# Performance work log

Hardware: AMD Instinct MI355X
Metric: run time of the kernel (lower is better)

Reference implementation:

```python
import jax, jax.numpy as jnp
import numpy as np

B, S, D, H = 2, 2048, 1024, 16
DK = D // H


def setup_inputs() -> dict:
    key = jax.random.key(0)
    ks = jax.random.split(key, 12)
    lim = 1.0 / np.sqrt(D)
    def lin(kw, kb):
        W = jax.random.uniform(kw, (D, D), jnp.float32, -lim, lim)
        b = jax.random.uniform(kb, (D,), jnp.float32, -lim, lim)
        return W, b
    Wq, bq = lin(ks[0], ks[1])
    Wk, bk = lin(ks[2], ks[3])
    Wv, bv = lin(ks[4], ks[5])
    Wo, bo = lin(ks[6], ks[7])
    Q = jax.random.normal(ks[8], (B, S, D), jnp.float32)
    K = jax.random.normal(ks[9], (B, S, D), jnp.float32)
    V = jax.random.normal(ks[10], (B, S, D), jnp.float32)
    # causal mask, broadcastable to (B, H, S, S)
    mask = jnp.broadcast_to(jnp.tril(jnp.ones((S, S), jnp.bool_))[None, None], (B, 1, S, S))
    return {"Q": Q, "K": K, "V": V, "mask": mask,
            "Wq": Wq, "bq": bq, "Wk": Wk, "bk": bk,
            "Wv": Wv, "bv": bv, "Wo": Wo, "bo": bo}


def reference(Q, K, V, mask, Wq, bq, Wk, bk, Wv, bv, Wo, bo):
    def split(x):  # (B,S,D) -> (B,H,S,DK)
        return x.reshape(B, S, H, DK).transpose(0, 2, 1, 3)
    q = split(Q @ Wq.T + bq)
    k = split(K @ Wk.T + bk)
    v = split(V @ Wv.T + bv)
    scores = jnp.einsum('bhqd,bhkd->bhqk', q, k) / jnp.sqrt(jnp.float32(DK))
    scores = jnp.where(mask, scores, jnp.float32(-1e9))
    probs = jax.nn.softmax(scores, axis=-1)
    out = jnp.einsum('bhqk,bhkd->bhqd', probs, v)  # (B,H,S,DK)
    out = out.transpose(0, 2, 1, 3).reshape(B, S, D)
    return out @ Wo.T + bo
```

## Files before the change

kernel.cpp:

```cpp
#include <hip/hip_runtime.h>

#define S_LEN 2048
#define D_DIM 1024
#define H_NUM 16
#define DK_DIM 64
#define BATCH 2
#define M_TOT (BATCH * S_LEN)
#define XSZ 4194304
#define WSZ 1048576
#define SCALE_LOG2 0.18033688f

typedef __bf16 bf16x8 __attribute__((ext_vector_type(8)));
typedef float f32x4 __attribute__((ext_vector_type(4)));
typedef unsigned short u16;

__device__ inline u16 f2bf(float f) {
  union { float f; unsigned u; } v; v.f = f;
  unsigned u = v.u;
  return (u16)((u + 0x7FFFu + ((u >> 16) & 1u)) >> 16);
}

typedef const __attribute__((address_space(1))) unsigned int gu32;
typedef __attribute__((address_space(3))) unsigned int lu32;
__device__ inline void glds16(const u16* g, u16* l) {
  __builtin_amdgcn_global_load_lds((gu32*)g, (lu32*)l, 16, 0, 0);
}

__global__ __launch_bounds__(256)
void convert_kernel(const float* __restrict__ Q, const float* __restrict__ K,
                    const float* __restrict__ V, const float* __restrict__ Wq,
                    const float* __restrict__ Wk, const float* __restrict__ Wv,
                    const float* __restrict__ Wo, u16* __restrict__ Xb,
                    u16* __restrict__ Wb) {
  const size_t e = ((size_t)blockIdx.x * 256 + threadIdx.x) * 8;
  const float* src;
  u16* dst;
  size_t off;
  if (e < 3ull * XSZ) {
    const int a = (int)(e >> 22);
    src = (a == 0) ? Q : (a == 1) ? K : V;
    off = e - ((size_t)a << 22);
    dst = Xb + e;
  } else {
    const size_t ew = e - 3ull * XSZ;
    const int a = (int)(ew >> 20);
    src = (a == 0) ? Wq : (a == 1) ? Wk : (a == 2) ? Wv : Wo;
    off = ew - ((size_t)a << 20);
    dst = Wb + ew;
  }
  const float4 v0 = *reinterpret_cast<const float4*>(&src[off]);
  const float4 v1 = *reinterpret_cast<const float4*>(&src[off + 4]);
  ushort4 w0, w1;
  w0.x = f2bf(v0.x); w0.y = f2bf(v0.y); w0.z = f2bf(v0.z); w0.w = f2bf(v0.w);
  w1.x = f2bf(v1.x); w1.y = f2bf(v1.y); w1.z = f2bf(v1.z); w1.w = f2bf(v1.w);
  *reinterpret_cast<ushort4*>(dst) = w0;
  *reinterpret_cast<ushort4*>(dst + 4) = w1;
}

template <int MODE>
__global__ __launch_bounds__(256)
void gemm_kernel(const u16* __restrict__ A0, const u16* __restrict__ B0,
                 const float* __restrict__ bias0, void* __restrict__ out0,
                 float scale0,
                 const u16* __restrict__ A1, const u16* __restrict__ B1,
                 const float* __restrict__ bias1, void* __restrict__ out1,
                 float scale1) {
  const u16* A = A0;
  const u16* Bw = B0;
  const float* bias = bias0;
  void* outp = out0;
  float oscale = scale0;
  if (MODE == 0 && blockIdx.z == 1) {
    A = A1; Bw = B1; bias = bias1; outp = out1; oscale = scale1;
  }

  __shared__ __align__(16) u16 Asm[128 * 64];
  __shared__ __align__(16) u16 Bsm[128 * 64];

  const int tid = threadIdx.x;
  const int m0 = blockIdx.x * 128, n0 = blockIdx.y * 128;
  const int wid = tid >> 6, lane = tid & 63;
  const int col = lane & 15, quad = lane >> 4;
  const int wm = (wid >> 1) * 64, wn = (wid & 1) * 64;

  const int lr = lane >> 3;
  const int lc = (lane & 7) ^ lr;
  const u16* gA = A + (size_t)(m0 + 32 * wid + lr) * D_DIM + lc * 8;
  const u16* gB = Bw + (size_t)(n0 + 32 * wid + lr) * D_DIM + lc * 8;

  f32x4 acc[4][4];
  const f32x4 zero4 = {0.f, 0.f, 0.f, 0.f};
  for (int i = 0; i < 4; i++)
    for (int j = 0; j < 4; j++) acc[i][j] = zero4;

  for (int k0 = 0; k0 < D_DIM; k0 += 64) {
    __syncthreads();
    for (int j = 0; j < 4; j++) {
      glds16(gA + (size_t)j * 8 * D_DIM + k0, &Asm[(32 * wid + 8 * j) * 64]);
      glds16(gB + (size_t)j * 8 * D_DIM + k0, &Bsm[(32 * wid + 8 * j) * 64]);
    }
    __syncthreads();

    bf16x8 af[4][2], bfm[4][2];
    for (int i = 0; i < 4; i++) {
      const int row = wm + i * 16 + col;
      const int r7 = row & 7;
      af[i][0] = *reinterpret_cast<const bf16x8*>(&Asm[row * 64 + ((quad ^ r7) * 8)]);
      af[i][1] = *reinterpret_cast<const bf16x8*>(&Asm[row * 64 + (((quad + 4) ^ r7) * 8)]);
    }
    for (int j = 0; j < 4; j++) {
      const int row = wn + j * 16 + col;
      const int r7 = row & 7;
      bfm[j][0] = *reinterpret_cast<const bf16x8*>(&Bsm[row * 64 + ((quad ^ r7) * 8)]);
      bfm[j][1] = *reinterpret_cast<const bf16x8*>(&Bsm[row * 64 + (((quad + 4) ^ r7) * 8)]);
    }
    for (int h = 0; h < 2; h++)
      for (int i = 0; i < 4; i++)
        for (int j = 0; j < 4; j++) {
          if (MODE == 1)
            acc[i][j] = __builtin_amdgcn_mfma_f32_16x16x32_bf16(
                af[i][h], bfm[j][h], acc[i][j], 0, 0, 0);
          else
            acc[i][j] = __builtin_amdgcn_mfma_f32_16x16x32_bf16(
                bfm[j][h], af[i][h], acc[i][j], 0, 0, 0);
        }
  }

  if (MODE == 0) {
    u16* out = (u16*)outp;
    float4 b4[4];
    for (int j = 0; j < 4; j++)
      b4[j] = *reinterpret_cast<const float4*>(&bias[n0 + wn + j * 16 + quad * 4]);
    for (int i = 0; i < 4; i++) {
      const int token = m0 + wm + i * 16 + col;
      const int b = token >> 11, s = token & (S_LEN - 1);
      for (int j = 0; j < 4; j++) {
        const int gnb = n0 + wn + j * 16 + quad * 4;
        const int h = gnb >> 6, dk = gnb & 63;
        ushort4 w;
        w.x = f2bf((acc[i][j][0] + b4[j].x) * oscale);
        w.y = f2bf((acc[i][j][1] + b4[j].y) * oscale);
        w.z = f2bf((acc[i][j][2] + b4[j].z) * oscale);
        w.w = f2bf((acc[i][j][3] + b4[j].w) * oscale);
        *reinterpret_cast<ushort4*>(
            &out[((size_t)(b * H_NUM + h) * S_LEN + s) * DK_DIM + dk]) = w;
      }
    }
  } else if (MODE == 1) {
    u16* out = (u16*)outp;
    float bb[4];
    for (int j = 0; j < 4; j++) bb[j] = bias[n0 + wn + j * 16 + col];
    for (int i = 0; i < 4; i++) {
      const int token0 = m0 + wm + i * 16 + quad * 4;
      const int b = token0 >> 11, s0 = token0 & (S_LEN - 1);
      for (int j = 0; j < 4; j++) {
        const int gn = n0 + wn + j * 16 + col;
        const int h = gn >> 6, dk = gn & 63;
        ushort4 w;
        w.x = f2bf(acc[i][j][0] + bb[j]);
        w.y = f2bf(acc[i][j][1] + bb[j]);
        w.z = f2bf(acc[i][j][2] + bb[j]);
        w.w = f2bf(acc[i][j][3] + bb[j]);
        *reinterpret_cast<ushort4*>(
            &out[((size_t)(b * H_NUM + h) * DK_DIM + dk) * S_LEN + s0]) = w;
      }
    }
  } else {
    float* out = (float*)outp;
    float4 b4[4];
    for (int j = 0; j < 4; j++)
      b4[j] = *reinterpret_cast<const float4*>(&bias[n0 + wn + j * 16 + quad * 4]);
    for (int i = 0; i < 4; i++) {
      const int token = m0 + wm + i * 16 + col;
      for (int j = 0; j < 4; j++) {
        const int gnb = n0 + wn + j * 16 + quad * 4;
        float4 v;
        v.x = acc[i][j][0] + b4[j].x;
        v.y = acc[i][j][1] + b4[j].y;
        v.z = acc[i][j][2] + b4[j].z;
        v.w = acc[i][j][3] + b4[j].w;
        *reinterpret_cast<float4*>(&out[(size_t)token * D_DIM + gnb]) = v;
      }
    }
  }
}

__global__ __launch_bounds__(256)
void attn_kernel(const u16* __restrict__ qh, const u16* __restrict__ kh,
                 const u16* __restrict__ vt, u16* __restrict__ ctx) {
  __shared__ __align__(16) u16 Ksm[64 * 64];
  __shared__ __align__(16) u16 Vsm[64 * 64];
  __shared__ __align__(16) u16 Psm[4][16][72];

  const int tid  = threadIdx.x;
  const int bh   = blockIdx.x;
  const int qb   = (bh & 16) ? (31 - blockIdx.y) : blockIdx.y;
  const int q0   = qb * 64;
  const int wid  = tid >> 6;
  const int lane = tid & 63;
  const int col  = lane & 15;
  const int quad = lane >> 4;
  const int qrow_w = q0 + wid * 16;
  const int qg     = qrow_w + col;

  bf16x8 qB[2];
  {
    const u16* qp = &qh[((size_t)bh * S_LEN + qg) * DK_DIM + quad * 8];
    qB[0] = *reinterpret_cast<const bf16x8*>(qp);
    qB[1] = *reinterpret_cast<const bf16x8*>(qp + 32);
  }

  float l_ = 0.f;
  f32x4 o[4];
  const f32x4 zero4 = {0.f, 0.f, 0.f, 0.f};
  for (int dm = 0; dm < 4; dm++) o[dm] = zero4;

  const int ntiles = qb + 1;
  const int lr = lane >> 3;
  const int lc = (lane & 7) ^ lr;
  const u16* kbase = kh + ((size_t)bh * S_LEN + 16 * wid + lr) * DK_DIM + lc * 8;
  const u16* vbase = vt + ((size_t)bh * DK_DIM + 16 * wid + lr) * S_LEN + lc * 8;
  const int r7 = col & 7;

  for (int t = 0; t < ntiles; t++) {
    const int kv0 = t * 64;
    __syncthreads();
    glds16(kbase + (size_t)kv0 * DK_DIM, &Ksm[(16 * wid) * 64]);
    glds16(kbase + (size_t)(kv0 + 8) * DK_DIM, &Ksm[(16 * wid + 8) * 64]);
    glds16(vbase + kv0, &Vsm[(16 * wid) * 64]);
    glds16(vbase + (size_t)8 * S_LEN + kv0, &Vsm[(16 * wid + 8) * 64]);
    __syncthreads();

    f32x4 s[4];
    for (int nc = 0; nc < 4; nc++) {
      const int row = nc * 16 + col;
      const bf16x8 kA0 = *reinterpret_cast<const bf16x8*>(
          &Ksm[row * 64 + (((quad) ^ r7) * 8)]);
      const bf16x8 kA1 = *reinterpret_cast<const bf16x8*>(
          &Ksm[row * 64 + (((quad + 4) ^ r7) * 8)]);
      f32x4 acc = zero4;
      acc = __builtin_amdgcn_mfma_f32_16x16x32_bf16(kA0, qB[0], acc, 0, 0, 0);
      acc = __builtin_amdgcn_mfma_f32_16x16x32_bf16(kA1, qB[1], acc, 0, 0, 0);
      s[nc] = acc;
    }

    ushort4 pk[4];
    const bool domask = (kv0 + 63 > qrow_w);
    if (domask) {
      for (int nc = 0; nc < 4; nc++) {
        const int kvb = kv0 + nc * 16 + quad * 4;
        float p[4];
        for (int r = 0; r < 4; r++) {
          const float e = __builtin_amdgcn_exp2f(s[nc][r]);
          p[r] = (kvb + r <= qg) ? e : 0.f;
          l_ += p[r];
        }
        pk[nc].x = f2bf(p[0]); pk[nc].y = f2bf(p[1]);
        pk[nc].z = f2bf(p[2]); pk[nc].w = f2bf(p[3]);
      }
    } else {
      for (int nc = 0; nc < 4; nc++) {
        float p[4];
        for (int r = 0; r < 4; r++) {
          p[r] = __builtin_amdgcn_exp2f(s[nc][r]);
          l_ += p[r];
        }
        pk[nc].x = f2bf(p[0]); pk[nc].y = f2bf(p[1]);
        pk[nc].z = f2bf(p[2]); pk[nc].w = f2bf(p[3]);
      }
    }
    for (int nc = 0; nc < 4; nc++)
      *reinterpret_cast<ushort4*>(&Psm[wid][col][nc * 16 + quad * 4]) = pk[nc];

    asm volatile("s_waitcnt lgkmcnt(0)" ::: "memory");

    bf16x8 pB[2];
    pB[0] = *reinterpret_cast<const bf16x8*>(&Psm[wid][col][quad * 8]);
    pB[1] = *reinterpret_cast<const bf16x8*>(&Psm[wid][col][32 + quad * 8]);
    for (int dm = 0; dm < 4; dm++) {
      const int row = dm * 16 + col;
      const bf16x8 vA0 = *reinterpret_cast<const bf16x8*>(
          &Vsm[row * 64 + (((quad) ^ r7) * 8)]);
      const bf16x8 vA1 = *reinterpret_cast<const bf16x8*>(
          &Vsm[row * 64 + (((quad + 4) ^ r7) * 8)]);
      o[dm] = __builtin_amdgcn_mfma_f32_16x16x32_bf16(vA0, pB[0], o[dm], 0, 0, 0);
      o[dm] = __builtin_amdgcn_mfma_f32_16x16x32_bf16(vA1, pB[1], o[dm], 0, 0, 0);
    }
  }

  float rs = l_;
  rs += __shfl_xor(rs, 16);
  rs += __shfl_xor(rs, 32);
  const float inv = 1.0f / rs;

  const int b = bh >> 4, h = bh & 15;
  for (int dm = 0; dm < 4; dm++) {
    ushort4 w;
    w.x = f2bf(o[dm][0] * inv);
    w.y = f2bf(o[dm][1] * inv);
    w.z = f2bf(o[dm][2] * inv);
    w.w = f2bf(o[dm][3] * inv);
    *reinterpret_cast<ushort4*>(
        &ctx[((size_t)b * S_LEN + qg) * D_DIM + h * DK_DIM + dm * 16 +
             quad * 4]) = w;
  }
}

extern "C" void kernel_launch(void* const* d_in, const int* in_sizes, int n_in,
                              void* d_out, int out_size, void* d_ws,
                              size_t ws_size, hipStream_t stream) {
  const float* Q  = (const float*)d_in[0];
  const float* K  = (const float*)d_in[1];
  const float* V  = (const float*)d_in[2];
  const float* Wq = (const float*)d_in[4];
  const float* bq = (const float*)d_in[5];
  const float* Wk = (const float*)d_in[6];
  const float* bk = (const float*)d_in[7];
  const float* Wv = (const float*)d_in[8];
  const float* bv = (const float*)d_in[9];
  const float* Wo = (const float*)d_in[10];
  const float* bo = (const float*)d_in[11];
  float* out = (float*)d_out;

  u16* qh  = (u16*)d_ws;
  u16* kh  = qh + XSZ;
  u16* vt  = kh + XSZ;
  u16* Qb  = vt + XSZ;
  u16* ctx = Qb;
  u16* Kb  = Qb + XSZ;
  u16* Vb  = Kb + XSZ;
  u16* Wqb = Vb + XSZ;
  u16* Wkb = Wqb + WSZ;
  u16* Wvb = Wkb + WSZ;
  u16* Wob = Wvb + WSZ;

  convert_kernel<<<(3 * XSZ + 4 * WSZ) / (256 * 8), 256, 0, stream>>>(
      Q, K, V, Wq, Wk, Wv, Wo, Qb, Wqb);

  gemm_kernel<0><<<dim3(M_TOT / 128, D_DIM / 128, 2), 256, 0, stream>>>(
      Qb, Wqb, bq, qh, SCALE_LOG2, Kb, Wkb, bk, kh, 1.0f);
  gemm_kernel<1><<<dim3(M_TOT / 128, D_DIM / 128, 1), 256, 0, stream>>>(
      Vb, Wvb, bv, vt, 1.0f, nullptr, nullptr, nullptr, nullptr, 1.0f);

  attn_kernel<<<dim3(BATCH * H_NUM, S_LEN / 64), 256, 0, stream>>>(qh, kh, vt,
                                                                   ctx);

  gemm_kernel<2><<<dim3(M_TOT / 128, D_DIM / 128, 1), 256, 0, stream>>>(
      ctx, Wob, bo, out, 1.0f, nullptr, nullptr, nullptr, nullptr, 1.0f);
}
```

Baseline: 243.9 us.

## Double-buffer K/V tiles and pair causal query blocks per attention workgroup

The attention kernel now double-buffers K and V tiles in LDS, issuing the next tile's global-to-LDS loads before computing on the current one, so the barrier-load-barrier stall per tile goes away. Each workgroup handles two query blocks (y and 31-y), which balances causal work and halves the grid to 512 blocks. Probability packing now uses byte-permute truncation to bf16, with the row sum built from the same truncated values instead of round-to-nearest. It costs double the K/V LDS, which may lower occupancy, and halves the number of resident blocks available to hide latency.

```diff
diff --git a/kernel.cpp b/kernel.cpp
--- a/kernel.cpp
+++ b/kernel.cpp
@@ -188,121 +188,133 @@
 __global__ __launch_bounds__(256)
 void attn_kernel(const u16* __restrict__ qh, const u16* __restrict__ kh,
                  const u16* __restrict__ vt, u16* __restrict__ ctx) {
-  __shared__ __align__(16) u16 Ksm[64 * 64];
-  __shared__ __align__(16) u16 Vsm[64 * 64];
+  __shared__ __align__(16) u16 Ksm[2][64 * 64];
+  __shared__ __align__(16) u16 Vsm[2][64 * 64];
   __shared__ __align__(16) u16 Psm[4][16][72];
 
   const int tid  = threadIdx.x;
   const int bh   = blockIdx.x;
-  const int qb   = (bh & 16) ? (31 - blockIdx.y) : blockIdx.y;
-  const int q0   = qb * 64;
+  const int y    = blockIdx.y;
   const int wid  = tid >> 6;
   const int lane = tid & 63;
   const int col  = lane & 15;
   const int quad = lane >> 4;
-  const int qrow_w = q0 + wid * 16;
-  const int qg     = qrow_w + col;
-
-  bf16x8 qB[2];
-  {
-    const u16* qp = &qh[((size_t)bh * S_LEN + qg) * DK_DIM + quad * 8];
-    qB[0] = *reinterpret_cast<const bf16x8*>(qp);
-    qB[1] = *reinterpret_cast<const bf16x8*>(qp + 32);
-  }
-
-  float l_ = 0.f;
-  f32x4 o[4];
-  const f32x4 zero4 = {0.f, 0.f, 0.f, 0.f};
-  for (int dm = 0; dm < 4; dm++) o[dm] = zero4;
-
-  const int ntiles = qb + 1;
+  const int r7   = col & 7;
+
   const int lr = lane >> 3;
   const int lc = (lane & 7) ^ lr;
   const u16* kbase = kh + ((size_t)bh * S_LEN + 16 * wid + lr) * DK_DIM + lc * 8;
   const u16* vbase = vt + ((size_t)bh * DK_DIM + 16 * wid + lr) * S_LEN + lc * 8;
-  const int r7 = col & 7;
-
-  for (int t = 0; t < ntiles; t++) {
-    const int kv0 = t * 64;
-    __syncthreads();
-    glds16(kbase + (size_t)kv0 * DK_DIM, &Ksm[(16 * wid) * 64]);
-    glds16(kbase + (size_t)(kv0 + 8) * DK_DIM, &Ksm[(16 * wid + 8) * 64]);
-    glds16(vbase + kv0, &Vsm[(16 * wid) * 64]);
-    glds16(vbase + (size_t)8 * S_LEN + kv0, &Vsm[(16 * wid + 8) * 64]);
-    __syncthreads();
-
-    f32x4 s[4];
-    for (int nc = 0; nc < 4; nc++) {
-      const int row = nc * 16 + col;
-      const bf16x8 kA0 = *reinterpret_cast<const bf16x8*>(
-          &Ksm[row * 64 + (((quad) ^ r7) * 8)]);
-      const bf16x8 kA1 = *reinterpret_cast<const bf16x8*>(
-          &Ksm[row * 64 + (((quad + 4) ^ r7) * 8)]);
-      f32x4 acc = zero4;
-      acc = __builtin_amdgcn_mfma_f32_16x16x32_bf16(kA0, qB[0], acc, 0, 0, 0);
-      acc = __builtin_amdgcn_mfma_f32_16x16x32_bf16(kA1, qB[1], acc, 0, 0, 0);
-      s[nc] = acc;
-    }
-
-    ushort4 pk[4];
-    const bool domask = (kv0 + 63 > qrow_w);
-    if (domask) {
+
+  const f32x4 zero4 = {0.f, 0.f, 0.f, 0.f};
+  const int b_ = bh >> 4, h_ = bh & 15;
+
+  glds16(kbase, &Ksm[0][(16 * wid) * 64]);
+  glds16(kbase + 8 * DK_DIM, &Ksm[0][(16 * wid + 8) * 64]);
+  glds16(vbase, &Vsm[0][(16 * wid) * 64]);
+  glds16(vbase + (size_t)8 * S_LEN, &Vsm[0][(16 * wid + 8) * 64]);
+
+  int t = 0;
+  for (int pp = 0; pp < 2; pp++) {
+    const int qb = pp ? (31 - y) : y;
+    const int nt = qb + 1;
+    const int qrow_w = qb * 64 + wid * 16;
+    const int qg = qrow_w + col;
+
+    bf16x8 qB[2];
+    {
+      const u16* qp = &qh[((size_t)bh * S_LEN + qg) * DK_DIM + quad * 8];
+      qB[0] = *reinterpret_cast<const bf16x8*>(qp);
+      qB[1] = *reinterpret_cast<const bf16x8*>(qp + 32);
+    }
+
+    float l_ = 0.f;
+    f32x4 o[4];
+    for (int dm = 0; dm < 4; dm++) o[dm] = zero4;
+
+    for (int tt = 0; tt < nt; tt++, t++) {
+      const int b = t & 1;
+      __syncthreads();
+
+      {
+        int nkv = -1;
+        if (tt + 1 < nt) nkv = (tt + 1) * 64;
+        else if (pp == 0) nkv = 0;
+        if (nkv >= 0) {
+          u16* kd = &Ksm[b ^ 1][(16 * wid) * 64];
+          u16* vd = &Vsm[b ^ 1][(16 * wid) * 64];
+          glds16(kbase + (size_t)nkv * DK_DIM, kd);
+          glds16(kbase + (size_t)(nkv + 8) * DK_DIM, kd + 8 * 64);
+          glds16(vbase + nkv, vd);
+          glds16(vbase + (size_t)8 * S_LEN + nkv, vd + 8 * 64);
+        }
+      }
+
+      const int kv0 = tt * 64;
+      f32x4 s[4];
+      for (int nc = 0; nc < 4; nc++) {
+        const int row = nc * 16 + col;
+        const bf16x8 kA0 = *reinterpret_cast<const bf16x8*>(
+            &Ksm[b][row * 64 + ((quad ^ r7) * 8)]);
+        const bf16x8 kA1 = *reinterpret_cast<const bf16x8*>(
+            &Ksm[b][row * 64 + (((quad + 4) ^ r7) * 8)]);
+        f32x4 acc = zero4;
+        acc = __builtin_amdgcn_mfma_f32_16x16x32_bf16(kA0, qB[0], acc, 0, 0, 0);
+        acc = __builtin_amdgcn_mfma_f32_16x16x32_bf16(kA1, qB[1], acc, 0, 0, 0);
+        s[nc] = acc;
+      }
+
+      const bool domask = (kv0 + 63 > qrow_w);
       for (int nc = 0; nc < 4; nc++) {
         const int kvb = kv0 + nc * 16 + quad * 4;
         float p[4];
         for (int r = 0; r < 4; r++) {
-          const float e = __builtin_amdgcn_exp2f(s[nc][r]);
-          p[r] = (kvb + r <= qg) ? e : 0.f;
-          l_ += p[r];
+          float e = __builtin_amdgcn_exp2f(s[nc][r]);
+          if (domask && (kvb + r > qg)) e = 0.f;
+          p[r] = e;
         }
-        pk[nc].x = f2bf(p[0]); pk[nc].y = f2bf(p[1]);
-        pk[nc].z = f2bf(p[2]); pk[nc].w = f2bf(p[3]);
-      }
-    } else {
-      for (int nc = 0; nc < 4; nc++) {
-        float p[4];
-        for (int r = 0; r < 4; r++) {
-          p[r] = __builtin_amdgcn_exp2f(s[nc][r]);
-          l_ += p[r];
-        }
-        pk[nc].x = f2bf(p[0]); pk[nc].y = f2bf(p[1]);
-        pk[nc].z = f2bf(p[2]); pk[nc].w = f2bf(p[3]);
-      }
-    }
-    for (int nc = 0; nc < 4; nc++)
-      *reinterpret_cast<ushort4*>(&Psm[wid][col][nc * 16 + quad * 4]) = pk[nc];
-
-    asm volatile("s_waitcnt lgkmcnt(0)" ::: "memory");
-
-    bf16x8 pB[2];
-    pB[0] = *reinterpret_cast<const bf16x8*>(&Psm[wid][col][quad * 8]);
-    pB[1] = *reinterpret_cast<const bf16x8*>(&Psm[wid][col][32 + quad * 8]);
+        unsigned u0 = __float_as_uint(p[0]), u1 = __float_as_uint(p[1]);
+        unsigned u2 = __float_as_uint(p[2]), u3 = __float_as_uint(p[3]);
+        l_ += __uint_as_float(u0 & 0xffff0000u);
+        l_ += __uint_as_float(u1 & 0xffff0000u);
+        l_ += __uint_as_float(u2 & 0xffff0000u);
+        l_ += __uint_as_float(u3 & 0xffff0000u);
+        uint2 pw;
+        pw.x = __builtin_amdgcn_perm(u1, u0, 0x07060302);
+        pw.y = __builtin_amdgcn_perm(u3, u2, 0x07060302);
+        *reinterpret_cast<uint2*>(&Psm[wid][col][nc * 16 + quad * 4]) = pw;
+      }
+
+      asm volatile("s_waitcnt lgkmcnt(0)" ::: "memory");
+
+      bf16x8 pB[2];
+      pB[0] = *reinterpret_cast<const bf16x8*>(&Psm[wid][col][quad * 8]);
+      pB[1] = *reinterpret_cast<const bf16x8*>(&Psm[wid][col][32 + quad * 8]);
+      for (int dm = 0; dm < 4; dm++) {
+        const int row = dm * 16 + col;
+        const bf16x8 vA0 = *reinterpret_cast<const bf16x8*>(
+            &Vsm[b][row * 64 + ((quad ^ r7) * 8)]);
+        const bf16x8 vA1 = *reinterpret_cast<const bf16x8*>(
+            &Vsm[b][row * 64 + (((quad + 4) ^ r7) * 8)]);
+        o[dm] = __builtin_amdgcn_mfma_f32_16x16x32_bf16(vA0, pB[0], o[dm], 0, 0, 0);
+        o[dm] = __builtin_amdgcn_mfma_f32_16x16x32_bf16(vA1, pB[1], o[dm], 0, 0, 0);
+      }
+    }
+
+    float rs = l_;
+    rs += __shfl_xor(rs, 16);
+    rs += __shfl_xor(rs, 32);
+    const float inv = 1.0f / rs;
     for (int dm = 0; dm < 4; dm++) {
-      const int row = dm * 16 + col;
-      const bf16x8 vA0 = *reinterpret_cast<const bf16x8*>(
-          &Vsm[row * 64 + (((quad) ^ r7) * 8)]);
-      const bf16x8 vA1 = *reinterpret_cast<const bf16x8*>(
-          &Vsm[row * 64 + (((quad + 4) ^ r7) * 8)]);
-      o[dm] = __builtin_amdgcn_mfma_f32_16x16x32_bf16(vA0, pB[0], o[dm], 0, 0, 0);
-      o[dm] = __builtin_amdgcn_mfma_f32_16x16x32_bf16(vA1, pB[1], o[dm], 0, 0, 0);
-    }
-  }
-
-  float rs = l_;
-  rs += __shfl_xor(rs, 16);
-  rs += __shfl_xor(rs, 32);
-  const float inv = 1.0f / rs;
-
-  const int b = bh >> 4, h = bh & 15;
-  for (int dm = 0; dm < 4; dm++) {
-    ushort4 w;
-    w.x = f2bf(o[dm][0] * inv);
-    w.y = f2bf(o[dm][1] * inv);
-    w.z = f2bf(o[dm][2] * inv);
-    w.w = f2bf(o[dm][3] * inv);
-    *reinterpret_cast<ushort4*>(
-        &ctx[((size_t)b * S_LEN + qg) * D_DIM + h * DK_DIM + dm * 16 +
-             quad * 4]) = w;
+      ushort4 w;
+      w.x = f2bf(o[dm][0] * inv);
+      w.y = f2bf(o[dm][1] * inv);
+      w.z = f2bf(o[dm][2] * inv);
+      w.w = f2bf(o[dm][3] * inv);
+      *reinterpret_cast<ushort4*>(
+          &ctx[((size_t)b_ * S_LEN + qg) * D_DIM + h_ * DK_DIM + dm * 16 +
+               quad * 4]) = w;
+    }
   }
 }
 
@@ -342,8 +354,7 @@
   gemm_kernel<1><<<dim3(M_TOT / 128, D_DIM / 128, 1), 256, 0, stream>>>(
       Vb, Wvb, bv, vt, 1.0f, nullptr, nullptr, nullptr, nullptr, 1.0f);
 
-  attn_kernel<<<dim3(BATCH * H_NUM, S_LEN / 64), 256, 0, stream>>>(qh, kh, vt,
-                                                                   ctx);
+  attn_kernel<<<dim3(BATCH * H_NUM, 16), 256, 0, stream>>>(qh, kh, vt, ctx);
 
   gemm_kernel<2><<<dim3(M_TOT / 128, D_DIM / 128, 1), 256, 0, stream>>>(
       ctx, Wob, bo, out, 1.0f, nullptr, nullptr, nullptr, nullptr, 1.0f);
```

After: 243.6 us. No clear change (-0.1%).
